# Optimization experiments

Measured on AMD Instinct MI355X. Metric: run time of the kernel, lower is better.

The kernel has to match this reference:

```python
import jax, jax.numpy as jnp
import numpy as np

N_NODES = 8192
N_UND = 65536      # undirected pairs placed
N_DIR = 131072     # extra directed edges placed


def _build_graph():
    rng = np.random.default_rng(0)
    A = np.zeros((N_NODES, N_NODES), np.float32)
    # undirected pairs (i<j), both directions set
    ii = rng.integers(0, N_NODES, 4 * N_UND)
    jj = rng.integers(0, N_NODES, 4 * N_UND)
    m = ii < jj
    iu, ju = ii[m][:N_UND], jj[m][:N_UND]
    A[iu, ju] = 1.0
    A[ju, iu] = 1.0
    # extra directed edges
    di = rng.integers(0, N_NODES, 2 * N_DIR)
    dj = rng.integers(0, N_NODES, 2 * N_DIR)
    m2 = di != dj
    A[di[m2][:N_DIR], dj[m2][:N_DIR]] = 1.0
    # dense_to_sparse: row, col of nonzeros
    row, col = np.nonzero(A)
    edge_index = np.stack([row, col]).astype(np.int32)
    # undirected mask: A==1 & A.T==1, upper triangle
    und = np.triu((A == 1.0) & (A.T == 1.0))
    u, v = np.nonzero(und)
    undirected_edges = np.stack([u, v], axis=1).astype(np.int32)
    return A, edge_index, undirected_edges


def setup_inputs() -> dict:
    key = jax.random.key(0)
    ks = jax.random.split(key, 4)
    A, edge_index, undirected_edges = _build_graph()
    N = N_NODES
    return {
        "adjacency": jnp.asarray(A),
        "W1": jax.random.normal(ks[0], (N, 16), jnp.float32) * 0.05,
        "b1": jnp.zeros((16,), jnp.float32),
        "W2": jax.random.normal(ks[1], (16, 8), jnp.float32) * 0.25,
        "b2": jnp.zeros((8,), jnp.float32),
        "Wfc": jax.random.normal(ks[2], (16, 1), jnp.float32) * 0.25,
        "bfc": jnp.zeros((1,), jnp.float32),
        "edge_index": jnp.asarray(edge_index),
        "undirected_edges": jnp.asarray(undirected_edges),
    }


def reference(adjacency, W1, b1, W2, b2, Wfc, bfc, edge_index, undirected_edges):
    N = adjacency.shape[0]
    src, dst = edge_index[0], edge_index[1]
    E = src.shape[0]
    # GCN normalization with self-loops (PyG gcn_norm): deg over target nodes
    deg = jax.ops.segment_sum(jnp.ones((E,), adjacency.dtype), dst,
                              num_segments=N) + 1.0
    dinv = jax.lax.rsqrt(deg)                       # deg >= 1, no inf
    norm = dinv[src] * dinv[dst]                    # [E]
    self_w = (dinv * dinv)[:, None]                 # self-loop coeff [N,1]

    def conv(h):  # h: [N, F] -> normalized scatter-add aggregation
        msg = norm[:, None] * h[src]                # [E, F]
        return jax.ops.segment_sum(msg, dst, num_segments=N) + self_w * h

    # node_features = eye(N), so eye(N) @ W1 == W1
    x = jax.nn.relu(conv(W1) + b1)                  # [N, 16]
    x = jax.nn.relu(conv(x @ W2) + b2)              # [N, 8]

    u, v = undirected_edges[:, 0], undirected_edges[:, 1]
    ef = jnp.concatenate([x[u], x[v]], axis=1)      # [U, 16]
    orient = jax.nn.sigmoid(ef @ Wfc + bfc)[:, 0]   # [U]

    out = adjacency.at[u, v].set(orient).at[v, u].set(1.0 - orient)
    return out
```

## Files before the change

### kernel.cpp

```cpp
#include <hip/hip_runtime.h>
#include <math.h>

#define F1 16
#define F2 8

__global__ void k_init_deg(float* __restrict__ deg, int N) {
    int i = blockIdx.x * blockDim.x + threadIdx.x;
    if (i < N) deg[i] = 1.0f;
}

__global__ void k_deg_accum(const int* __restrict__ dst, float* __restrict__ deg, int E) {
    int e = blockIdx.x * blockDim.x + threadIdx.x;
    if (e < E) atomicAdd(&deg[dst[e]], 1.0f);
}

__global__ void k_dinv_initx1(const float* __restrict__ deg, float* __restrict__ dinv,
                              const float* __restrict__ W1, float* __restrict__ x1, int N) {
    int i = blockIdx.x * blockDim.x + threadIdx.x;
    if (i < N) {
        float di = rsqrtf(deg[i]);
        dinv[i] = di;
        float sw = di * di;
        #pragma unroll
        for (int f = 0; f < F1; ++f)
            x1[i * F1 + f] = sw * W1[i * F1 + f];
    }
}

__global__ void k_conv1_edges(const int* __restrict__ src, const int* __restrict__ dst,
                              const float* __restrict__ dinv, const float* __restrict__ W1,
                              float* __restrict__ x1, int E) {
    int id = blockIdx.x * blockDim.x + threadIdx.x;
    int e = id >> 4;
    int f = id & (F1 - 1);
    if (e < E) {
        int s = src[e], d = dst[e];
        float nrm = dinv[s] * dinv[d];
        atomicAdd(&x1[d * F1 + f], nrm * W1[s * F1 + f]);
    }
}

__global__ void k_layer1_finish(const float* __restrict__ dinv, const float* __restrict__ b1,
                                const float* __restrict__ W2, const float* __restrict__ x1,
                                float* __restrict__ h2, float* __restrict__ x2, int N) {
    int i = blockIdx.x * blockDim.x + threadIdx.x;
    if (i < N) {
        float r[F1];
        #pragma unroll
        for (int f = 0; f < F1; ++f) {
            float v = x1[i * F1 + f] + b1[f];
            r[f] = v > 0.0f ? v : 0.0f;
        }
        float di = dinv[i];
        float sw = di * di;
        #pragma unroll
        for (int g = 0; g < F2; ++g) {
            float acc = 0.0f;
            #pragma unroll
            for (int f = 0; f < F1; ++f)
                acc += r[f] * W2[f * F2 + g];
            h2[i * F2 + g] = acc;
            x2[i * F2 + g] = sw * acc;
        }
    }
}

__global__ void k_conv2_edges(const int* __restrict__ src, const int* __restrict__ dst,
                              const float* __restrict__ dinv, const float* __restrict__ h2,
                              float* __restrict__ x2, int E) {
    int id = blockIdx.x * blockDim.x + threadIdx.x;
    int e = id >> 3;
    int g = id & (F2 - 1);
    if (e < E) {
        int s = src[e], d = dst[e];
        float nrm = dinv[s] * dinv[d];
        atomicAdd(&x2[d * F2 + g], nrm * h2[s * F2 + g]);
    }
}

__global__ void k_fill_zero(float4* __restrict__ o, long n4) {
    long i = (long)blockIdx.x * blockDim.x + threadIdx.x;
    if (i < n4) o[i] = make_float4(0.f, 0.f, 0.f, 0.f);
}

__global__ void k_scatter_ones(const int* __restrict__ src, const int* __restrict__ dst,
                               float* __restrict__ out, int E, int N) {
    int e = blockIdx.x * blockDim.x + threadIdx.x;
    if (e < E) {
        out[(long)src[e] * N + dst[e]] = 1.0f;
    }
}

__global__ void k_orient(const int2* __restrict__ ue, const float* __restrict__ x2,
                         const float* __restrict__ b2, const float* __restrict__ Wfc,
                         const float* __restrict__ bfc, float* __restrict__ out,
                         int U, int N) {
    int k = blockIdx.x * blockDim.x + threadIdx.x;
    if (k < U) {
        int2 e = ue[k];
        int u = e.x, v = e.y;
        float s = bfc[0];
        #pragma unroll
        for (int g = 0; g < F2; ++g) {
            float xu = x2[u * F2 + g] + b2[g];
            float xv = x2[v * F2 + g] + b2[g];
            xu = xu > 0.0f ? xu : 0.0f;
            xv = xv > 0.0f ? xv : 0.0f;
            s += xu * Wfc[g] + xv * Wfc[F2 + g];
        }
        float orient = 1.0f / (1.0f + expf(-s));
        out[(long)u * N + v] = orient;
        out[(long)v * N + u] = 1.0f - orient;
    }
}

extern "C" void kernel_launch(void* const* d_in, const int* in_sizes, int n_in,
                              void* d_out, int out_size, void* d_ws, size_t ws_size,
                              hipStream_t stream) {
    const float* W1  = (const float*)d_in[1];
    const float* b1  = (const float*)d_in[2];
    const float* W2  = (const float*)d_in[3];
    const float* b2  = (const float*)d_in[4];
    const float* Wfc = (const float*)d_in[5];
    const float* bfc = (const float*)d_in[6];
    const int* edge_index = (const int*)d_in[7];
    const int* und        = (const int*)d_in[8];

    int N = in_sizes[1] / F1;
    int E = in_sizes[7] / 2;
    int U = in_sizes[8] / 2;
    const int* src = edge_index;
    const int* dst = edge_index + E;

    float* ws   = (float*)d_ws;
    float* deg  = ws;
    float* dinv = ws + N;
    float* x1   = ws + 2 * N;
    float* h2   = x1 + (long)F1 * N;
    float* x2   = h2 + (long)F2 * N;

    const int B = 256;

    {
        long n4 = (long)N * N / 4;
        long blocks = (n4 + B - 1) / B;
        k_fill_zero<<<(int)blocks, B, 0, stream>>>((float4*)d_out, n4);
    }
    k_scatter_ones<<<(E + B - 1) / B, B, 0, stream>>>(src, dst, (float*)d_out, E, N);

    k_init_deg<<<(N + B - 1) / B, B, 0, stream>>>(deg, N);
    k_deg_accum<<<(E + B - 1) / B, B, 0, stream>>>(dst, deg, E);
    k_dinv_initx1<<<(N + B - 1) / B, B, 0, stream>>>(deg, dinv, W1, x1, N);

    {
        long work = (long)E * F1;
        k_conv1_edges<<<(int)((work + B - 1) / B), B, 0, stream>>>(src, dst, dinv, W1, x1, E);
    }
    k_layer1_finish<<<(N + B - 1) / B, B, 0, stream>>>(dinv, b1, W2, x1, h2, x2, N);

    {
        long work = (long)E * F2;
        k_conv2_edges<<<(int)((work + B - 1) / B), B, 0, stream>>>(src, dst, dinv, h2, x2, E);
    }

    k_orient<<<(U + B - 1) / B, B, 0, stream>>>((const int2*)und, x2, b2, Wfc, bfc,
                                                (float*)d_out, U, N);
}
```

Before: 455.5 us.

## Replace fill kernel with memset, fuse scatter with degree, defer self-loop terms

Zeroing the 256 MB output is now done with hipMemsetAsync instead of a custom float4 kernel. A single memset also zeroes deg, x1 and x2, which removes the init kernels. The ones-scatter is fused with degree accumulation. The self-loop contributions (sw*W1 and sw*h2) move into the consumer kernels, so the accumulators can start from zero and fewer launches are needed. The memset path may or may not beat the custom fill, and the orient kernel now reads extra h2 and dinv values.

Result: no change. 451.3 us (-0.9%).

```diff
diff --git a/kernel.cpp b/kernel.cpp
--- a/kernel.cpp
+++ b/kernel.cpp
@@ -4,27 +4,20 @@
 #define F1 16
 #define F2 8
 
-__global__ void k_init_deg(float* __restrict__ deg, int N) {
-    int i = blockIdx.x * blockDim.x + threadIdx.x;
-    if (i < N) deg[i] = 1.0f;
+__global__ void k_edges0(const int* __restrict__ src, const int* __restrict__ dst,
+                         float* __restrict__ out, float* __restrict__ deg,
+                         int E, int N) {
+    int e = blockIdx.x * blockDim.x + threadIdx.x;
+    if (e < E) {
+        int s = src[e], d = dst[e];
+        out[(long)s * N + d] = 1.0f;
+        atomicAdd(&deg[d], 1.0f);
+    }
 }
 
-__global__ void k_deg_accum(const int* __restrict__ dst, float* __restrict__ deg, int E) {
-    int e = blockIdx.x * blockDim.x + threadIdx.x;
-    if (e < E) atomicAdd(&deg[dst[e]], 1.0f);
-}
-
-__global__ void k_dinv_initx1(const float* __restrict__ deg, float* __restrict__ dinv,
-                              const float* __restrict__ W1, float* __restrict__ x1, int N) {
+__global__ void k_dinv(const float* __restrict__ deg, float* __restrict__ dinv, int N) {
     int i = blockIdx.x * blockDim.x + threadIdx.x;
-    if (i < N) {
-        float di = rsqrtf(deg[i]);
-        dinv[i] = di;
-        float sw = di * di;
-        #pragma unroll
-        for (int f = 0; f < F1; ++f)
-            x1[i * F1 + f] = sw * W1[i * F1 + f];
-    }
+    if (i < N) dinv[i] = rsqrtf(deg[i] + 1.0f);
 }
 
 __global__ void k_conv1_edges(const int* __restrict__ src, const int* __restrict__ dst,
@@ -40,19 +33,19 @@
     }
 }
 
-__global__ void k_layer1_finish(const float* __restrict__ dinv, const float* __restrict__ b1,
-                                const float* __restrict__ W2, const float* __restrict__ x1,
-                                float* __restrict__ h2, float* __restrict__ x2, int N) {
+__global__ void k_layer1(const float* __restrict__ dinv, const float* __restrict__ b1,
+                         const float* __restrict__ W1, const float* __restrict__ W2,
+                         const float* __restrict__ x1, float* __restrict__ h2, int N) {
     int i = blockIdx.x * blockDim.x + threadIdx.x;
     if (i < N) {
+        float di = dinv[i];
+        float sw = di * di;
         float r[F1];
         #pragma unroll
         for (int f = 0; f < F1; ++f) {
-            float v = x1[i * F1 + f] + b1[f];
+            float v = x1[i * F1 + f] + sw * W1[i * F1 + f] + b1[f];
             r[f] = v > 0.0f ? v : 0.0f;
         }
-        float di = dinv[i];
-        float sw = di * di;
         #pragma unroll
         for (int g = 0; g < F2; ++g) {
             float acc = 0.0f;
@@ -60,7 +53,6 @@
             for (int f = 0; f < F1; ++f)
                 acc += r[f] * W2[f * F2 + g];
             h2[i * F2 + g] = acc;
-            x2[i * F2 + g] = sw * acc;
         }
     }
 }
@@ -78,20 +70,8 @@
     }
 }
 
-__global__ void k_fill_zero(float4* __restrict__ o, long n4) {
-    long i = (long)blockIdx.x * blockDim.x + threadIdx.x;
-    if (i < n4) o[i] = make_float4(0.f, 0.f, 0.f, 0.f);
-}
-
-__global__ void k_scatter_ones(const int* __restrict__ src, const int* __restrict__ dst,
-                               float* __restrict__ out, int E, int N) {
-    int e = blockIdx.x * blockDim.x + threadIdx.x;
-    if (e < E) {
-        out[(long)src[e] * N + dst[e]] = 1.0f;
-    }
-}
-
 __global__ void k_orient(const int2* __restrict__ ue, const float* __restrict__ x2,
+                         const float* __restrict__ h2, const float* __restrict__ dinv,
                          const float* __restrict__ b2, const float* __restrict__ Wfc,
                          const float* __restrict__ bfc, float* __restrict__ out,
                          int U, int N) {
@@ -99,11 +79,13 @@
     if (k < U) {
         int2 e = ue[k];
         int u = e.x, v = e.y;
+        float swu = dinv[u] * dinv[u];
+        float swv = dinv[v] * dinv[v];
         float s = bfc[0];
         #pragma unroll
         for (int g = 0; g < F2; ++g) {
-            float xu = x2[u * F2 + g] + b2[g];
-            float xv = x2[v * F2 + g] + b2[g];
+            float xu = x2[u * F2 + g] + swu * h2[u * F2 + g] + b2[g];
+            float xv = x2[v * F2 + g] + swv * h2[v * F2 + g] + b2[g];
             xu = xu > 0.0f ? xu : 0.0f;
             xv = xv > 0.0f ? xv : 0.0f;
             s += xu * Wfc[g] + xv * Wfc[F2 + g];
@@ -134,35 +116,31 @@
 
     float* ws   = (float*)d_ws;
     float* deg  = ws;
-    float* dinv = ws + N;
-    float* x1   = ws + 2 * N;
-    float* h2   = x1 + (long)F1 * N;
-    float* x2   = h2 + (long)F2 * N;
+    float* x1   = ws + N;
+    float* x2   = x1 + (long)F1 * N;
+    float* dinv = x2 + (long)F2 * N;
+    float* h2   = dinv + N;
 
     const int B = 256;
 
-    {
-        long n4 = (long)N * N / 4;
-        long blocks = (n4 + B - 1) / B;
-        k_fill_zero<<<(int)blocks, B, 0, stream>>>((float4*)d_out, n4);
-    }
-    k_scatter_ones<<<(E + B - 1) / B, B, 0, stream>>>(src, dst, (float*)d_out, E, N);
+    hipMemsetAsync(d_out, 0, (size_t)N * N * sizeof(float), stream);
+    hipMemsetAsync(d_ws, 0, (size_t)(N + (long)F1 * N + (long)F2 * N) * sizeof(float), stream);
 
-    k_init_deg<<<(N + B - 1) / B, B, 0, stream>>>(deg, N);
-    k_deg_accum<<<(E + B - 1) / B, B, 0, stream>>>(dst, deg, E);
-    k_dinv_initx1<<<(N + B - 1) / B, B, 0, stream>>>(deg, dinv, W1, x1, N);
+    k_edges0<<<(E + B - 1) / B, B, 0, stream>>>(src, dst, (float*)d_out, deg, E, N);
+
+    k_dinv<<<(N + B - 1) / B, B, 0, stream>>>(deg, dinv, N);
 
     {
         long work = (long)E * F1;
         k_conv1_edges<<<(int)((work + B - 1) / B), B, 0, stream>>>(src, dst, dinv, W1, x1, E);
     }
-    k_layer1_finish<<<(N + B - 1) / B, B, 0, stream>>>(dinv, b1, W2, x1, h2, x2, N);
+    k_layer1<<<(N + B - 1) / B, B, 0, stream>>>(dinv, b1, W1, W2, x1, h2, N);
 
     {
         long work = (long)E * F2;
         k_conv2_edges<<<(int)((work + B - 1) / B), B, 0, stream>>>(src, dst, dinv, h2, x2, E);
     }
 
-    k_orient<<<(U + B - 1) / B, B, 0, stream>>>((const int2*)und, x2, b2, Wfc, bfc,
+    k_orient<<<(U + B - 1) / B, B, 0, stream>>>((const int2*)und, x2, h2, dinv, b2, Wfc, bfc,
                                                 (float*)d_out, U, N);
 }
```
